# Performance work log

Measured on AMD Instinct MI355X. Metric: run time of the kernel, lower is better.

## Reference

```python
import jax, jax.numpy as jnp
import numpy as np

EMBED_DIM = 1024
Q_DIM = 512
KV_DIM = 512
NUM_HEADS = 16
HEAD_DIM = EMBED_DIM // NUM_HEADS
EPS = 1e-5


def setup_inputs() -> dict:
    key = jax.random.key(0)
    ks = jax.random.split(key, 13)
    B, N1, N2 = 2, 2048, 2048
    s_q = 1.0 / np.sqrt(Q_DIM)
    s_kv = 1.0 / np.sqrt(KV_DIM)
    s_e = 1.0 / np.sqrt(EMBED_DIM)
    return {
        "query": jax.random.normal(ks[0], (B, N1, Q_DIM), jnp.float32),
        "key": jax.random.normal(ks[1], (B, N2, KV_DIM), jnp.float32),
        "value": jax.random.normal(ks[2], (B, N2, KV_DIM), jnp.float32),
        "Wq": jax.random.uniform(ks[3], (Q_DIM, EMBED_DIM), jnp.float32, -s_q, s_q),
        "bq": jax.random.uniform(ks[4], (EMBED_DIM,), jnp.float32, -s_q, s_q),
        "Wk": jax.random.uniform(ks[5], (KV_DIM, EMBED_DIM), jnp.float32, -s_kv, s_kv),
        "bk": jax.random.uniform(ks[6], (EMBED_DIM,), jnp.float32, -s_kv, s_kv),
        "Wv": jax.random.uniform(ks[7], (KV_DIM, EMBED_DIM), jnp.float32, -s_kv, s_kv),
        "bv": jax.random.uniform(ks[8], (EMBED_DIM,), jnp.float32, -s_kv, s_kv),
        "Wo": jax.random.uniform(ks[9], (EMBED_DIM, EMBED_DIM), jnp.float32, -s_e, s_e),
        "bo": jax.random.uniform(ks[10], (EMBED_DIM,), jnp.float32, -s_e, s_e),
        "gamma": jnp.ones((EMBED_DIM,), jnp.float32),
        "beta": jnp.zeros((EMBED_DIM,), jnp.float32),
    }


def reference(query, key, value, Wq, bq, Wk, bk, Wv, bv, Wo, bo, gamma, beta):
    B, N1, _ = query.shape
    _, N2, _ = key.shape
    scale = HEAD_DIM ** (-0.5)
    # projections -> [B, H, N, D]
    Q = (query @ Wq + bq).reshape(B, N1, NUM_HEADS, HEAD_DIM).transpose(0, 2, 1, 3)
    K = (key @ Wk + bk).reshape(B, N2, NUM_HEADS, HEAD_DIM).transpose(0, 2, 1, 3)
    V = (value @ Wv + bv).reshape(B, N2, NUM_HEADS, HEAD_DIM).transpose(0, 2, 1, 3)
    # full score matrix [B, H, N1, N2] (matches original eager attention)
    att = jnp.einsum("bhqd,bhkd->bhqk", Q, K) * scale
    att = jax.nn.softmax(att, axis=-1)
    # dropout is identity in eval mode
    out = jnp.einsum("bhqk,bhkd->bhqd", att, V)  # [B, H, N1, D]
    out = out.transpose(0, 2, 1, 3).reshape(B, N1, EMBED_DIM)
    out = out @ Wo + bo
    # LayerNorm
    mu = out.mean(-1, keepdims=True)
    var = ((out - mu) ** 2).mean(-1, keepdims=True)
    return (out - mu) * jax.lax.rsqrt(var + EPS) * gamma + beta
```

## Files before the change

### kernel.cpp

```cpp
#include <hip/hip_runtime.h>

typedef __bf16 bf16x8 __attribute__((ext_vector_type(8)));
typedef __bf16 bf16x4 __attribute__((ext_vector_type(4)));
typedef float f32x4 __attribute__((ext_vector_type(4)));
typedef short s16x4 __attribute__((ext_vector_type(4)));
typedef unsigned short u16;
typedef unsigned int u32;

__device__ __forceinline__ f32x4 mfma16(bf16x8 a, bf16x8 b, f32x4 c) {
  return __builtin_amdgcn_mfma_f32_16x16x32_bf16(a, b, c, 0, 0, 0);
}

__device__ __forceinline__ f32x4 mfma16k16(bf16x4 a, bf16x4 b, f32x4 c) {
#if __has_builtin(__builtin_amdgcn_mfma_f32_16x16x16bf16_1k)
  union { bf16x4 bf; s16x4 s; } ua, ub;
  ua.bf = a; ub.bf = b;
  return __builtin_amdgcn_mfma_f32_16x16x16bf16_1k(ua.s, ub.s, c, 0, 0, 0);
#elif __has_builtin(__builtin_amdgcn_mfma_f32_16x16x16_bf16)
  return __builtin_amdgcn_mfma_f32_16x16x16_bf16(a, b, c, 0, 0, 0);
#else
  asm("v_mfma_f32_16x16x16_bf16 %0, %1, %2, %0" : "+v"(c) : "v"(a), "v"(b));
  return c;
#endif
}

__device__ __forceinline__ void gload_lds16(const void* g, void* l) {
  __builtin_amdgcn_global_load_lds(
      (const __attribute__((address_space(1))) void*)g,
      (__attribute__((address_space(3))) void*)l, 16, 0, 0);
}

__global__ __launch_bounds__(256) void tobf16_3(const float4* __restrict__ a,
                                                const float4* __restrict__ b,
                                                const float4* __restrict__ c,
                                                bf16x4* __restrict__ oa,
                                                bf16x4* __restrict__ ob,
                                                bf16x4* __restrict__ oc, int n4) {
  int i = blockIdx.x * 256 + threadIdx.x;
  if (i >= n4) return;
  const int z = blockIdx.y;
  const float4* in = z == 0 ? a : z == 1 ? b : c;
  bf16x4* out = z == 0 ? oa : z == 1 ? ob : oc;
  float4 v = in[i];
  bf16x4 o;
  o[0] = (__bf16)v.x; o[1] = (__bf16)v.y; o[2] = (__bf16)v.z; o[3] = (__bf16)v.w;
  out[i] = o;
}

__global__ __launch_bounds__(256) void wtrans4(const float* __restrict__ W0,
                                               const float* __restrict__ W1,
                                               const float* __restrict__ W2,
                                               const float* __restrict__ W3,
                                               u16* __restrict__ T0, u16* __restrict__ T1,
                                               u16* __restrict__ T2, u16* __restrict__ T3) {
  const int z = blockIdx.z;
  const int K = (z == 3) ? 1024 : 512;
  const int N = 1024;
  const int k0 = blockIdx.y * 32;
  if (k0 >= K) return;
  const float* W = z == 0 ? W0 : z == 1 ? W1 : z == 2 ? W2 : W3;
  u16* Wt = z == 0 ? T0 : z == 1 ? T1 : z == 2 ? T2 : T3;
  __shared__ float t[32][33];
  const int tx = threadIdx.x, ty = threadIdx.y;
  const int n0 = blockIdx.x * 32;
#pragma unroll
  for (int i = 0; i < 4; ++i)
    t[ty + i * 8][tx] = W[(size_t)(k0 + ty + i * 8) * N + n0 + tx];
  __syncthreads();
#pragma unroll
  for (int i = 0; i < 4; ++i)
    ((__bf16*)Wt)[(size_t)(n0 + ty + i * 8) * K + k0 + tx] = (__bf16)t[tx][ty + i * 8];
}

template <int MODE, int DBUF>
__device__ __forceinline__ void gemm_body(const u16* __restrict__ A,
                                          const u16* __restrict__ Bt,
                                          const float* __restrict__ bias,
                                          void* __restrict__ Cout,
                                          int M, int N, int K, float scl) {
  constexpr int NB = DBUF ? 2 : 1;
  __shared__ __align__(16) u16 lA[NB][128 * 64];
  __shared__ __align__(16) u16 lB[NB][128 * 64];
  const int tid = threadIdx.x;
  const int w = tid >> 6, l = tid & 63;
  const int li = l & 15, lg = l >> 4;
  const int wm = w & 1, wn = w >> 1;
  const int bm = blockIdx.x * 128, bn = blockIdx.y * 128;

  f32x4 acc[4][4] = {};
  const int nk = K >> 6;

  auto stage = [&](int kt, int bufi) {
    const int k0 = kt << 6;
#pragma unroll
    for (int i = 0; i < 4; ++i) {
      const int c0 = (i * 4 + w) * 64;
      const int f = c0 + l;
      const int r = f >> 3, cs = (f & 7) ^ (r & 7);
      gload_lds16(A + (size_t)(bm + r) * K + k0 + cs * 8, &lA[bufi][c0 * 8]);
      gload_lds16(Bt + (size_t)(bn + r) * K + k0 + cs * 8, &lB[bufi][c0 * 8]);
    }
  };

  int cur = 0;
  if (DBUF) {
    stage(0, 0);
    __syncthreads();
  }

  for (int kt = 0; kt < nk; ++kt) {
    if (DBUF) {
      if (kt + 1 < nk) stage(kt + 1, cur ^ 1);
    } else {
      stage(kt, 0);
      __syncthreads();
    }
    bf16x8 af[4][2], bfr[4][2];
#pragma unroll
    for (int m = 0; m < 4; ++m) {
      const int row = wm * 64 + m * 16 + li;
#pragma unroll
      for (int kk = 0; kk < 2; ++kk) {
        const int kc = (lg + kk * 4) ^ (row & 7);
        af[m][kk] = *(const bf16x8*)&lA[cur][row * 64 + kc * 8];
      }
    }
#pragma unroll
    for (int n = 0; n < 4; ++n) {
      const int row = wn * 64 + n * 16 + li;
#pragma unroll
      for (int kk = 0; kk < 2; ++kk) {
        const int kc = (lg + kk * 4) ^ (row & 7);
        bfr[n][kk] = *(const bf16x8*)&lB[cur][row * 64 + kc * 8];
      }
    }
#pragma unroll
    for (int m = 0; m < 4; ++m)
#pragma unroll
      for (int n = 0; n < 4; ++n) {
        acc[m][n] = mfma16(af[m][0], bfr[n][0], acc[m][n]);
        acc[m][n] = mfma16(af[m][1], bfr[n][1], acc[m][n]);
      }
    __syncthreads();
    if (DBUF) cur ^= 1;
  }

#pragma unroll
  for (int m = 0; m < 4; ++m) {
    const int row0 = bm + wm * 64 + m * 16 + lg * 4;
#pragma unroll
    for (int n = 0; n < 4; ++n) {
      const int col = bn + wn * 64 + n * 16 + li;
      const float bv = bias[col];
      if (MODE == 2) {
        const int bq = row0 >> 11, kv = row0 & 2047;
        bf16x4 pk;
#pragma unroll
        for (int r = 0; r < 4; ++r) pk[r] = (__bf16)((acc[m][n][r] + bv) * scl);
        *(bf16x4*)&((u16*)Cout)[((size_t)(bq * 1024 + col)) * 2048 + kv] = pk;
      } else {
#pragma unroll
        for (int r = 0; r < 4; ++r) {
          float v = (acc[m][n][r] + bv) * scl;
          ((__bf16*)Cout)[(size_t)(row0 + r) * N + col] = (__bf16)v;
        }
      }
    }
  }
}

__global__ __launch_bounds__(256) void gemm_qkv(const u16* __restrict__ xq,
                                                const u16* __restrict__ xk,
                                                const u16* __restrict__ xv,
                                                const u16* __restrict__ wqt,
                                                const u16* __restrict__ wkt,
                                                const u16* __restrict__ wvt,
                                                const float* __restrict__ bq,
                                                const float* __restrict__ bk,
                                                const float* __restrict__ bv,
                                                u16* __restrict__ Qb, u16* __restrict__ Kb,
                                                u16* __restrict__ Vt, float qscale) {
  const int z = blockIdx.z;
  if (z == 0) {
    gemm_body<0, 0>(xq, wqt, bq, Qb, 4096, 1024, 512, qscale);
  } else if (z == 1) {
    gemm_body<0, 0>(xk, wkt, bk, Kb, 4096, 1024, 512, 1.0f);
  } else {
    gemm_body<2, 0>(xv, wvt, bv, Vt, 4096, 1024, 512, 1.0f);
  }
}

__global__ __launch_bounds__(256) void gemm_o(const u16* __restrict__ A,
                                              const u16* __restrict__ Bt,
                                              const float* __restrict__ bias,
                                              u16* __restrict__ C) {
  gemm_body<0, 1>(A, Bt, bias, C, 4096, 1024, 1024, 1.0f);
}

__global__ __launch_bounds__(512) void attn64(const u16* __restrict__ Qb,
                                              const u16* __restrict__ Kb,
                                              const u16* __restrict__ Vt,
                                              u16* __restrict__ Ob,
                                              int N1, int N2) {
  const int tid = threadIdx.x;
  const int w = tid >> 6, l = tid & 63;
  const int li = l & 15, lg = l >> 4;

  const int flat = blockIdx.x + 16 * (blockIdx.y + 16 * blockIdx.z);
  const int xcd = flat & 7, idx = flat >> 3;
  const int qb = idx & 15, pr = idx >> 4;
  const int h = 2 * xcd + (pr & 1);
  const int b = pr >> 1;
  const int q0 = qb * 128;

  __shared__ __align__(16) u16 lK[2][64 * 64];
  __shared__ __align__(16) u16 lV[2][64 * 64];

  const size_t qoff = (size_t)(b * N1 + q0 + w * 16 + li) * 1024 + h * 64;
  const bf16x8 qa0 = *(const bf16x8*)&Qb[qoff + lg * 8];
  const bf16x8 qa1 = *(const bf16x8*)&Qb[qoff + 32 + lg * 8];

  const u16* Kbase = Kb + (size_t)b * N2 * 1024 + h * 64;
  const u16* Vbase = Vt + (size_t)((b * 16 + h) * 64) * N2;

  const int sr = tid >> 3;
  const int sc = (tid & 7) ^ (sr & 7);

  f32x4 o[4] = {};
  float lsum = 0.f;
  const int li7 = li & 7;
  const int ca = lg ^ li7, cb = (lg + 4) ^ li7;
  const int vsub = (lg & 1) * 4;
  const int lgh = lg >> 1;

  const int nt = N2 >> 6;
  int cur = 0;
  gload_lds16(Kbase + (size_t)sr * 1024 + sc * 8, &lK[0][w * 512]);
  gload_lds16(Vbase + (size_t)sr * N2 + sc * 8, &lV[0][w * 512]);
  __syncthreads();

  for (int t = 0; t < nt; ++t) {
    if (t + 1 < nt) {
      gload_lds16(Kbase + (size_t)((t + 1) * 64 + sr) * 1024 + sc * 8, &lK[cur ^ 1][w * 512]);
      gload_lds16(Vbase + (size_t)sr * N2 + (t + 1) * 64 + sc * 8, &lV[cur ^ 1][w * 512]);
    }
    const u16* K_ = lK[cur];
    const u16* V_ = lV[cur];

    float s_t = 0.f;
    bf16x4 pk[4];
    __builtin_amdgcn_s_setprio(1);
#pragma unroll
    for (int n = 0; n < 4; ++n) {
      const int row = n * 16 + li;
      bf16x8 k0 = *(const bf16x8*)&K_[row * 64 + ca * 8];
      bf16x8 k1 = *(const bf16x8*)&K_[row * 64 + cb * 8];
      f32x4 a = {};
      a = mfma16(k0, qa0, a);
      a = mfma16(k1, qa1, a);
      float p0 = __builtin_amdgcn_exp2f(a[0]);
      float p1 = __builtin_amdgcn_exp2f(a[1]);
      float p2 = __builtin_amdgcn_exp2f(a[2]);
      float p3 = __builtin_amdgcn_exp2f(a[3]);
      s_t += (p0 + p1) + (p2 + p3);
      pk[n][0] = (__bf16)p0; pk[n][1] = (__bf16)p1;
      pk[n][2] = (__bf16)p2; pk[n][3] = (__bf16)p3;
    }
    __builtin_amdgcn_s_setprio(0);
    lsum += s_t;

    __builtin_amdgcn_s_setprio(1);
#pragma unroll
    for (int n = 0; n < 4; ++n) {
      const int c0 = ((2 * n + lgh) ^ li7) * 8 + vsub;
#pragma unroll
      for (int dt = 0; dt < 4; ++dt) {
        const int row = dt * 16 + li;
        const bf16x4 vf = *(const bf16x4*)&V_[row * 64 + c0];
        o[dt] = mfma16k16(vf, pk[n], o[dt]);
      }
    }
    __builtin_amdgcn_s_setprio(0);
    __syncthreads();
    cur ^= 1;
  }

  lsum += __shfl_xor(lsum, 16, 64);
  lsum += __shfl_xor(lsum, 32, 64);
  const float inv = 1.f / lsum;

  const size_t orow = (size_t)(b * N1 + q0 + w * 16 + li) * 1024 + h * 64;
#pragma unroll
  for (int dt = 0; dt < 4; ++dt) {
    bf16x4 pkk;
#pragma unroll
    for (int r = 0; r < 4; ++r) pkk[r] = (__bf16)(o[dt][r] * inv);
    *(bf16x4*)&Ob[orow + dt * 16 + lg * 4] = pkk;
  }
}

__global__ __launch_bounds__(256) void lnorm(const u16* __restrict__ X,
                                             const float* __restrict__ gamma,
                                             const float* __restrict__ beta,
                                             float* __restrict__ out) {
  const int row = blockIdx.x;
  const int tid = threadIdx.x;
  const bf16x4 xv = ((const bf16x4*)(X + (size_t)row * 1024))[tid];
  float4 v;
  v.x = (float)xv[0]; v.y = (float)xv[1]; v.z = (float)xv[2]; v.w = (float)xv[3];
  float s = v.x + v.y + v.z + v.w;
  float sq = v.x * v.x + v.y * v.y + v.z * v.z + v.w * v.w;
#pragma unroll
  for (int d = 1; d < 64; d <<= 1) {
    s += __shfl_xor(s, d, 64);
    sq += __shfl_xor(sq, d, 64);
  }
  __shared__ float red[8];
  const int w = tid >> 6, l = tid & 63;
  if (l == 0) { red[w] = s; red[4 + w] = sq; }
  __syncthreads();
  s = red[0] + red[1] + red[2] + red[3];
  sq = red[4] + red[5] + red[6] + red[7];
  const float mu = s * (1.f / 1024.f);
  const float var = sq * (1.f / 1024.f) - mu * mu;
  const float rstd = rsqrtf(var + 1e-5f);
  const float4 g = ((const float4*)gamma)[tid];
  const float4 bb = ((const float4*)beta)[tid];
  float4 o;
  o.x = (v.x - mu) * rstd * g.x + bb.x;
  o.y = (v.y - mu) * rstd * g.y + bb.y;
  o.z = (v.z - mu) * rstd * g.z + bb.z;
  o.w = (v.w - mu) * rstd * g.w + bb.w;
  ((float4*)(out + (size_t)row * 1024))[tid] = o;
}

extern "C" void kernel_launch(void* const* d_in, const int* in_sizes, int n_in,
                              void* d_out, int out_size, void* d_ws, size_t ws_size,
                              hipStream_t stream) {
  const float* query = (const float*)d_in[0];
  const float* key_ = (const float*)d_in[1];
  const float* value = (const float*)d_in[2];
  const float* Wq = (const float*)d_in[3];
  const float* bq = (const float*)d_in[4];
  const float* Wk = (const float*)d_in[5];
  const float* bk = (const float*)d_in[6];
  const float* Wv = (const float*)d_in[7];
  const float* bv = (const float*)d_in[8];
  const float* Wo = (const float*)d_in[9];
  const float* bo = (const float*)d_in[10];
  const float* gamma = (const float*)d_in[11];
  const float* beta = (const float*)d_in[12];

  constexpr int B = 2, N1 = 2048, N2 = 2048, E = 1024, QKD = 512;
  constexpr int M = B * N1;
  const float QSCALE = 0.125f * 1.4426950408889634f;

  char* p = (char*)d_ws;
  auto alloc = [&](size_t bytes) {
    char* r = p;
    p += (bytes + 255) & ~(size_t)255;
    return r;
  };
  u16* xq = (u16*)alloc((size_t)M * QKD * 2);
  u16* xk = (u16*)alloc((size_t)M * QKD * 2);
  u16* xv = (u16*)alloc((size_t)M * QKD * 2);
  u16* wqt = (u16*)alloc((size_t)E * QKD * 2);
  u16* wkt = (u16*)alloc((size_t)E * QKD * 2);
  u16* wvt = (u16*)alloc((size_t)E * QKD * 2);
  u16* wot = (u16*)alloc((size_t)E * E * 2);
  u16* Qb = (u16*)alloc((size_t)M * E * 2);
  u16* Kb = (u16*)alloc((size_t)M * E * 2);
  u16* Vt = (u16*)alloc((size_t)M * E * 2);
  u16* ao = (u16*)alloc((size_t)M * E * 2);
  u16* ao2 = (u16*)alloc((size_t)M * E * 2);

  const int n4 = M * QKD / 4;
  tobf16_3<<<dim3((n4 + 255) / 256, 3), 256, 0, stream>>>(
      (const float4*)query, (const float4*)key_, (const float4*)value,
      (bf16x4*)xq, (bf16x4*)xk, (bf16x4*)xv, n4);

  wtrans4<<<dim3(E / 32, 32, 4), dim3(32, 8), 0, stream>>>(
      Wq, Wk, Wv, Wo, wqt, wkt, wvt, wot);

  gemm_qkv<<<dim3(M / 128, E / 128, 3), 256, 0, stream>>>(
      xq, xk, xv, wqt, wkt, wvt, bq, bk, bv, Qb, Kb, Vt, QSCALE);

  attn64<<<dim3(16, 16, B), 512, 0, stream>>>(Qb, Kb, Vt, ao, N1, N2);

  gemm_o<<<dim3(M / 128, E / 128), 256, 0, stream>>>(ao, wot, bo, ao2);

  lnorm<<<M, 256, 0, stream>>>(ao2, gamma, beta, (float*)d_out);
}
```

Before: 115.6 us.

## Switch attention to 32x32x16 MFMA with 4 waves and LDS-staged P

Rewrites the attention kernel to use 32x32x16 bf16 MFMA tiles, with each of 4 waves owning 32 query rows instead of 8 waves owning 16 rows each. The softmax probabilities are written to a per-wave swizzled LDS buffer and read back as the B operand of the P·V product, replacing the 16x16x16 MFMA path that used register-held P. This aims for higher MFMA throughput per instruction and fewer K/V LDS reads per FLOP. In exchange it adds LDS traffic and usage for P, uses fewer threads per block, and keeps 32-wide accumulators live, which raises register pressure.

```diff
diff --git a/kernel.cpp b/kernel.cpp
--- a/kernel.cpp
+++ b/kernel.cpp
@@ -3,7 +3,7 @@
 typedef __bf16 bf16x8 __attribute__((ext_vector_type(8)));
 typedef __bf16 bf16x4 __attribute__((ext_vector_type(4)));
 typedef float f32x4 __attribute__((ext_vector_type(4)));
-typedef short s16x4 __attribute__((ext_vector_type(4)));
+typedef float f32x16 __attribute__((ext_vector_type(16)));
 typedef unsigned short u16;
 typedef unsigned int u32;
 
@@ -11,17 +11,8 @@
   return __builtin_amdgcn_mfma_f32_16x16x32_bf16(a, b, c, 0, 0, 0);
 }
 
-__device__ __forceinline__ f32x4 mfma16k16(bf16x4 a, bf16x4 b, f32x4 c) {
-#if __has_builtin(__builtin_amdgcn_mfma_f32_16x16x16bf16_1k)
-  union { bf16x4 bf; s16x4 s; } ua, ub;
-  ua.bf = a; ub.bf = b;
-  return __builtin_amdgcn_mfma_f32_16x16x16bf16_1k(ua.s, ub.s, c, 0, 0, 0);
-#elif __has_builtin(__builtin_amdgcn_mfma_f32_16x16x16_bf16)
-  return __builtin_amdgcn_mfma_f32_16x16x16_bf16(a, b, c, 0, 0, 0);
-#else
-  asm("v_mfma_f32_16x16x16_bf16 %0, %1, %2, %0" : "+v"(c) : "v"(a), "v"(b));
-  return c;
-#endif
+__device__ __forceinline__ f32x16 mfma32(bf16x8 a, bf16x8 b, f32x16 c) {
+  return __builtin_amdgcn_mfma_f32_32x32x16_bf16(a, b, c, 0, 0, 0);
 }
 
 __device__ __forceinline__ void gload_lds16(const void* g, void* l) {
@@ -197,14 +188,14 @@
   gemm_body<0, 1>(A, Bt, bias, C, 4096, 1024, 1024, 1.0f);
 }
 
-__global__ __launch_bounds__(512) void attn64(const u16* __restrict__ Qb,
+__global__ __launch_bounds__(256) void attn64(const u16* __restrict__ Qb,
                                               const u16* __restrict__ Kb,
                                               const u16* __restrict__ Vt,
                                               u16* __restrict__ Ob,
                                               int N1, int N2) {
   const int tid = threadIdx.x;
   const int w = tid >> 6, l = tid & 63;
-  const int li = l & 15, lg = l >> 4;
+  const int q = l & 31, hi = l >> 5;
 
   const int flat = blockIdx.x + 16 * (blockIdx.y + 16 * blockIdx.z);
   const int xcd = flat & 7, idx = flat >> 3;
@@ -215,69 +206,87 @@
 
   __shared__ __align__(16) u16 lK[2][64 * 64];
   __shared__ __align__(16) u16 lV[2][64 * 64];
-
-  const size_t qoff = (size_t)(b * N1 + q0 + w * 16 + li) * 1024 + h * 64;
-  const bf16x8 qa0 = *(const bf16x8*)&Qb[qoff + lg * 8];
-  const bf16x8 qa1 = *(const bf16x8*)&Qb[qoff + 32 + lg * 8];
+  __shared__ __align__(16) u16 lP[4][32 * 64];
+
+  const size_t qoff = (size_t)(b * N1 + q0 + w * 32 + q) * 1024 + h * 64;
+  bf16x8 qa[4];
+#pragma unroll
+  for (int dk = 0; dk < 4; ++dk)
+    qa[dk] = *(const bf16x8*)&Qb[qoff + dk * 16 + hi * 8];
 
   const u16* Kbase = Kb + (size_t)b * N2 * 1024 + h * 64;
   const u16* Vbase = Vt + (size_t)((b * 16 + h) * 64) * N2;
 
-  const int sr = tid >> 3;
-  const int sc = (tid & 7) ^ (sr & 7);
-
-  f32x4 o[4] = {};
+  const int sr0 = w * 8 + (l >> 3);
+  const int sc0 = (l & 7) ^ (sr0 & 7);
+  const int sr1 = 32 + sr0;
+  const int sc1 = (l & 7) ^ (sr1 & 7);
+  const int d0 = w * 512, d1 = 2048 + w * 512;
+
+  f32x16 o0 = {}, o1 = {};
   float lsum = 0.f;
-  const int li7 = li & 7;
-  const int ca = lg ^ li7, cb = (lg + 4) ^ li7;
-  const int vsub = (lg & 1) * 4;
-  const int lgh = lg >> 1;
+  u16* lPw = &lP[w][0];
+  const int q7 = q & 7;
 
   const int nt = N2 >> 6;
   int cur = 0;
-  gload_lds16(Kbase + (size_t)sr * 1024 + sc * 8, &lK[0][w * 512]);
-  gload_lds16(Vbase + (size_t)sr * N2 + sc * 8, &lV[0][w * 512]);
+  gload_lds16(Kbase + (size_t)sr0 * 1024 + sc0 * 8, &lK[0][d0]);
+  gload_lds16(Kbase + (size_t)sr1 * 1024 + sc1 * 8, &lK[0][d1]);
+  gload_lds16(Vbase + (size_t)sr0 * N2 + sc0 * 8, &lV[0][d0]);
+  gload_lds16(Vbase + (size_t)sr1 * N2 + sc1 * 8, &lV[0][d1]);
   __syncthreads();
 
   for (int t = 0; t < nt; ++t) {
     if (t + 1 < nt) {
-      gload_lds16(Kbase + (size_t)((t + 1) * 64 + sr) * 1024 + sc * 8, &lK[cur ^ 1][w * 512]);
-      gload_lds16(Vbase + (size_t)sr * N2 + (t + 1) * 64 + sc * 8, &lV[cur ^ 1][w * 512]);
+      const int kv1 = (t + 1) * 64;
+      gload_lds16(Kbase + (size_t)(kv1 + sr0) * 1024 + sc0 * 8, &lK[cur ^ 1][d0]);
+      gload_lds16(Kbase + (size_t)(kv1 + sr1) * 1024 + sc1 * 8, &lK[cur ^ 1][d1]);
+      gload_lds16(Vbase + (size_t)sr0 * N2 + kv1 + sc0 * 8, &lV[cur ^ 1][d0]);
+      gload_lds16(Vbase + (size_t)sr1 * N2 + kv1 + sc1 * 8, &lV[cur ^ 1][d1]);
     }
     const u16* K_ = lK[cur];
     const u16* V_ = lV[cur];
 
     float s_t = 0.f;
-    bf16x4 pk[4];
     __builtin_amdgcn_s_setprio(1);
 #pragma unroll
-    for (int n = 0; n < 4; ++n) {
-      const int row = n * 16 + li;
-      bf16x8 k0 = *(const bf16x8*)&K_[row * 64 + ca * 8];
-      bf16x8 k1 = *(const bf16x8*)&K_[row * 64 + cb * 8];
-      f32x4 a = {};
-      a = mfma16(k0, qa0, a);
-      a = mfma16(k1, qa1, a);
-      float p0 = __builtin_amdgcn_exp2f(a[0]);
-      float p1 = __builtin_amdgcn_exp2f(a[1]);
-      float p2 = __builtin_amdgcn_exp2f(a[2]);
-      float p3 = __builtin_amdgcn_exp2f(a[3]);
-      s_t += (p0 + p1) + (p2 + p3);
-      pk[n][0] = (__bf16)p0; pk[n][1] = (__bf16)p1;
-      pk[n][2] = (__bf16)p2; pk[n][3] = (__bf16)p3;
+    for (int kvsub = 0; kvsub < 2; ++kvsub) {
+      const int row = kvsub * 32 + q;
+      const int r7 = row & 7;
+      f32x16 a = {};
+#pragma unroll
+      for (int dk = 0; dk < 4; ++dk) {
+        const bf16x8 kf = *(const bf16x8*)&K_[row * 64 + ((2 * dk + hi) ^ r7) * 8];
+        a = mfma32(kf, qa[dk], a);
+      }
+#pragma unroll
+      for (int g = 0; g < 4; ++g) {
+        float p0 = __builtin_amdgcn_exp2f(a[4 * g + 0]);
+        float p1 = __builtin_amdgcn_exp2f(a[4 * g + 1]);
+        float p2 = __builtin_amdgcn_exp2f(a[4 * g + 2]);
+        float p3 = __builtin_amdgcn_exp2f(a[4 * g + 3]);
+        s_t += (p0 + p1) + (p2 + p3);
+        bf16x4 pk;
+        pk[0] = (__bf16)p0; pk[1] = (__bf16)p1; pk[2] = (__bf16)p2; pk[3] = (__bf16)p3;
+        *(bf16x4*)&lPw[q * 64 + (((4 * kvsub + g) ^ q7) << 3) + 4 * hi] = pk;
+      }
     }
     __builtin_amdgcn_s_setprio(0);
     lsum += s_t;
 
     __builtin_amdgcn_s_setprio(1);
 #pragma unroll
-    for (int n = 0; n < 4; ++n) {
-      const int c0 = ((2 * n + lgh) ^ li7) * 8 + vsub;
-#pragma unroll
-      for (int dt = 0; dt < 4; ++dt) {
-        const int row = dt * 16 + li;
-        const bf16x4 vf = *(const bf16x4*)&V_[row * 64 + c0];
-        o[dt] = mfma16k16(vf, pk[n], o[dt]);
+    for (int ks = 0; ks < 4; ++ks) {
+      const bf16x8 pf = *(const bf16x8*)&lPw[q * 64 + (((2 * ks + hi) ^ q7) << 3)];
+      {
+        const int row = q;
+        const bf16x8 vf = *(const bf16x8*)&V_[row * 64 + ((2 * ks + hi) ^ (row & 7)) * 8];
+        o0 = mfma32(vf, pf, o0);
+      }
+      {
+        const int row = 32 + q;
+        const bf16x8 vf = *(const bf16x8*)&V_[row * 64 + ((2 * ks + hi) ^ (row & 7)) * 8];
+        o1 = mfma32(vf, pf, o1);
       }
     }
     __builtin_amdgcn_s_setprio(0);
@@ -285,17 +294,20 @@
     cur ^= 1;
   }
 
-  lsum += __shfl_xor(lsum, 16, 64);
   lsum += __shfl_xor(lsum, 32, 64);
   const float inv = 1.f / lsum;
 
-  const size_t orow = (size_t)(b * N1 + q0 + w * 16 + li) * 1024 + h * 64;
-#pragma unroll
-  for (int dt = 0; dt < 4; ++dt) {
-    bf16x4 pkk;
-#pragma unroll
-    for (int r = 0; r < 4; ++r) pkk[r] = (__bf16)(o[dt][r] * inv);
-    *(bf16x4*)&Ob[orow + dt * 16 + lg * 4] = pkk;
+  const size_t orow = (size_t)(b * N1 + q0 + w * 32 + q) * 1024 + h * 64;
+#pragma unroll
+  for (int g = 0; g < 4; ++g) {
+    bf16x4 pk0, pk1;
+#pragma unroll
+    for (int r = 0; r < 4; ++r) {
+      pk0[r] = (__bf16)(o0[4 * g + r] * inv);
+      pk1[r] = (__bf16)(o1[4 * g + r] * inv);
+    }
+    *(bf16x4*)&Ob[orow + 8 * g + 4 * hi] = pk0;
+    *(bf16x4*)&Ob[orow + 32 + 8 * g + 4 * hi] = pk1;
   }
 }
 
@@ -385,7 +397,7 @@
   gemm_qkv<<<dim3(M / 128, E / 128, 3), 256, 0, stream>>>(
       xq, xk, xv, wqt, wkt, wvt, bq, bk, bv, Qb, Kb, Vt, QSCALE);
 
-  attn64<<<dim3(16, 16, B), 512, 0, stream>>>(Qb, Kb, Vt, ao, N1, N2);
+  attn64<<<dim3(16, 16, B), 256, 0, stream>>>(Qb, Kb, Vt, ao, N1, N2);
 
   gemm_o<<<dim3(M / 128, E / 128), 256, 0, stream>>>(ao, wot, bo, ao2);
 
```

Measured after the change: 117.6 us. No clear change (+1.7%).
